# Kernel optimization log

Hardware: AMD Instinct MI355X
Metric: run time of the kernel (lower is better)

## Reference

```python
import jax, jax.numpy as jnp
import numpy as np

G, N, E = 4, 50000, 800000
F_IN, HID, OUT = 64, 128, 64


def setup_inputs() -> dict:
    key = jax.random.key(0)
    ks = jax.random.split(key, 4)
    x = jax.random.normal(ks[0], (G, N, F_IN), dtype=jnp.float32)
    edge_index = jax.random.randint(ks[1], (G, 2, E), 0, N)
    W1 = jax.random.normal(ks[2], (G, F_IN, HID), dtype=jnp.float32) / np.sqrt(F_IN).astype(np.float32)
    b1 = jnp.zeros((G, HID), dtype=jnp.float32)
    W2 = jax.random.normal(ks[3], (G, HID, OUT), dtype=jnp.float32) / np.sqrt(HID).astype(np.float32)
    b2 = jnp.zeros((G, OUT), dtype=jnp.float32)
    return {"x": x, "edge_index": edge_index, "W1": W1, "b1": b1, "W2": W2, "b2": b2}


def gcn_conv(x, src, dst, W, b):
    # PyG GCNConv: add self loops, symmetric norm D^-1/2 (A+I) D^-1/2, then XW + b
    n = x.shape[0]
    loop = jnp.arange(n)
    s = jnp.concatenate([src, loop])  # [E+N]
    d = jnp.concatenate([dst, loop])
    deg = jax.ops.segment_sum(jnp.ones_like(s, dtype=x.dtype), d, num_segments=n)
    dinv = jax.lax.rsqrt(deg)  # deg >= 1 because of self loops
    norm = dinv[s] * dinv[d]  # [E+N]
    h = x @ W  # [N, F_out]
    msg = h[s] * norm[:, None]  # edge-wise gather (memory-bound)
    out = jax.ops.segment_sum(msg, d, num_segments=n)  # scatter-add
    return out + b


def reference(x, edge_index, W1, b1, W2, b2):
    def per_graph(xg, eg, w1, b1g, w2, b2g):
        src, dst = eg[0], eg[1]
        h = jax.nn.elu(gcn_conv(xg, src, dst, w1, b1g))
        h = jax.nn.elu(gcn_conv(h, src, dst, w2, b2g))
        return h  # [N, OUT]

    out = jax.vmap(per_graph)(x, edge_index, W1, b1, W2, b2)  # [G, N, OUT]
    return out.reshape(G * N, OUT)  # torch.cat over graphs along dim 0
```

## Files before the change

### kernel.cpp

```cpp
#include <hip/hip_runtime.h>
#include <cstdint>

constexpr int G = 4, N = 50000, E = 800000;
constexpr int FIN = 64, HID = 128, FOUT = 64;
constexpr int NB = (N + 1023) / 1024;

constexpr int PB = 64;
constexpr int CP = E / PB;
constexpr int NBK = (N + 255) / 256;

typedef unsigned short ushort;
typedef _Float16 f16;

__device__ __forceinline__ ushort f2h(float f) {
  f16 h = (f16)f;
  return __builtin_bit_cast(ushort, h);
}
__device__ __forceinline__ float h2f(ushort u) {
  f16 h = __builtin_bit_cast(f16, u);
  return (float)h;
}

__device__ __forceinline__ void xcd_map(int b, int& g, int& chunk) {
  int xcd = b & 7;
  int sub = b >> 3;
  g = xcd >> 1;
  chunk = (xcd & 1) * 6250 + sub;
}

__global__ void k_x2h(const float4* __restrict__ X, ushort4* __restrict__ Xh, int n4) {
  int i = blockIdx.x * blockDim.x + threadIdx.x;
  if (i >= n4) return;
  float4 v = X[i];
  ushort4 o = {f2h(v.x), f2h(v.y), f2h(v.z), f2h(v.w)};
  Xh[i] = o;
}


__global__ __launch_bounds__(256) void k_phist(const int* __restrict__ ei,
                                               int* __restrict__ PH) {
  __shared__ int h[NBK];
  int pb = blockIdx.x, g = blockIdx.y;
  for (int i = threadIdx.x; i < NBK; i += 256) h[i] = 0;
  __syncthreads();
  const int4* dst4 = (const int4*)(ei + (size_t)g * 2 * E + E + (size_t)pb * CP);
  for (int i = threadIdx.x; i < CP / 4; i += 256) {
    int4 d = dst4[i];
    atomicAdd(&h[d.x >> 8], 1);
    atomicAdd(&h[d.y >> 8], 1);
    atomicAdd(&h[d.z >> 8], 1);
    atomicAdd(&h[d.w >> 8], 1);
  }
  __syncthreads();
  for (int i = threadIdx.x; i < NBK; i += 256)
    PH[((size_t)g * NBK + i) * PB + pb] = h[i];
}

__global__ void k_pscan(const int* __restrict__ PH, int* __restrict__ POFF,
                        int* __restrict__ BB) {
  int g = blockIdx.x, k = threadIdx.x;
  int tot = 0;
  if (k < NBK) {
#pragma unroll 8
    for (int pb = 0; pb < PB; ++pb) tot += PH[((size_t)g * NBK + k) * PB + pb];
  }
  __shared__ int sm[256];
  sm[k] = tot;
  __syncthreads();
  for (int off = 1; off < 256; off <<= 1) {
    int v = (k >= off) ? sm[k - off] : 0;
    __syncthreads();
    sm[k] += v;
    __syncthreads();
  }
  int excl = sm[k] - tot;
  if (k < NBK) {
    BB[g * (NBK + 1) + k] = excl;
    if (k == NBK - 1) BB[g * (NBK + 1) + NBK] = excl + tot;
    int run = excl;
#pragma unroll 8
    for (int pb = 0; pb < PB; ++pb) {
      POFF[((size_t)g * NBK + k) * PB + pb] = run;
      run += PH[((size_t)g * NBK + k) * PB + pb];
    }
  }
}

__global__ __launch_bounds__(256) void k_part(const int* __restrict__ ei,
                                              const int* __restrict__ POFF,
                                              unsigned* __restrict__ pairs) {
  __shared__ int off[NBK];
  __shared__ int rk[NBK];
  int pb = blockIdx.x, g = blockIdx.y;
  for (int i = threadIdx.x; i < NBK; i += 256) {
    off[i] = POFF[((size_t)g * NBK + i) * PB + pb];
    rk[i] = 0;
  }
  __syncthreads();
  const int* base = ei + (size_t)g * 2 * E + (size_t)pb * CP;
  const int4* s4 = (const int4*)base;
  const int4* d4 = (const int4*)(base + E);
  unsigned* pg = pairs + (size_t)g * E;
  for (int i = threadIdx.x; i < CP / 4; i += 256) {
    int4 s = s4[i], d = d4[i];
    int sv[4] = {s.x, s.y, s.z, s.w};
    int dv[4] = {d.x, d.y, d.z, d.w};
#pragma unroll
    for (int k = 0; k < 4; ++k) {
      int b = dv[k] >> 8;
      int r = atomicAdd(&rk[b], 1);
      pg[off[b] + r] = (unsigned)sv[k] | ((unsigned)(dv[k] & 255) << 16);
    }
  }
}

__global__ __launch_bounds__(256) void k_bcnt(const unsigned* __restrict__ pairs,
                                              const int* __restrict__ BB,
                                              int* __restrict__ cnt) {
  __shared__ int h[256];
  int k = blockIdx.x, g = blockIdx.y;
  h[threadIdx.x] = 0;
  __syncthreads();
  int lo = BB[g * (NBK + 1) + k], hi = BB[g * (NBK + 1) + k + 1];
  const unsigned* pg = pairs + (size_t)g * E;
  for (int i = lo + (int)threadIdx.x; i < hi; i += 256)
    atomicAdd(&h[(pg[i] >> 16) & 255], 1);
  __syncthreads();
  int n0 = k << 8;
  int nn = min(256, N - n0);
  if ((int)threadIdx.x < nn) cnt[g * N + n0 + threadIdx.x] = h[threadIdx.x];
}

__global__ __launch_bounds__(256) void k_place(const unsigned* __restrict__ pairs,
                                               const int* __restrict__ BB,
                                               const int* __restrict__ rowptr,
                                               int* __restrict__ col) {
  __shared__ int rp[256];
  __shared__ int rk[256];
  int k = blockIdx.x, g = blockIdx.y;
  int n0 = k << 8;
  int nn = min(256, N - n0);
  if ((int)threadIdx.x < nn) rp[threadIdx.x] = rowptr[g * (N + 1) + n0 + threadIdx.x];
  rk[threadIdx.x] = 0;
  __syncthreads();
  int lo = BB[g * (NBK + 1) + k], hi = BB[g * (NBK + 1) + k + 1];
  const unsigned* pg = pairs + (size_t)g * E;
  int* cg = col + (size_t)g * E;
  for (int i = lo + (int)threadIdx.x; i < hi; i += 256) {
    unsigned p = pg[i];
    int dl = (p >> 16) & 255;
    int r = atomicAdd(&rk[dl], 1);
    cg[rp[dl] + r] = (int)(p & 0xffffu);
  }
}

__global__ void k_scan_partial(const int* __restrict__ cnt, int* __restrict__ part) {
  int g = blockIdx.y, b = blockIdx.x, tid = threadIdx.x;
  int base = b * 1024 + tid * 4;
  int s = 0;
#pragma unroll
  for (int k = 0; k < 4; ++k) {
    int i = base + k;
    if (i < N) s += cnt[g * N + i];
  }
  __shared__ int sm[256];
  sm[tid] = s;
  __syncthreads();
  for (int off = 128; off > 0; off >>= 1) {
    if (tid < off) sm[tid] += sm[tid + off];
    __syncthreads();
  }
  if (tid == 0) part[g * NB + b] = sm[0];
}

__global__ void k_scan_mid(int* __restrict__ part, int* __restrict__ rowptr) {
  int g = blockIdx.x;
  if (threadIdx.x != 0) return;
  int run = 0;
  for (int b = 0; b < NB; ++b) {
    int t = part[g * NB + b];
    part[g * NB + b] = run;
    run += t;
  }
  rowptr[g * (N + 1) + N] = run;
}

__global__ void k_scan_final(const int* __restrict__ cnt, const int* __restrict__ part,
                             int* __restrict__ rowptr, float* __restrict__ dinv) {
  int g = blockIdx.y, b = blockIdx.x, tid = threadIdx.x;
  int base = b * 1024 + tid * 4;
  int c[4];
  int s = 0;
#pragma unroll
  for (int k = 0; k < 4; ++k) {
    int i = base + k;
    c[k] = (i < N) ? cnt[g * N + i] : 0;
    s += c[k];
  }
  __shared__ int sm[256];
  sm[tid] = s;
  __syncthreads();
  for (int off = 1; off < 256; off <<= 1) {
    int v = (tid >= off) ? sm[tid - off] : 0;
    __syncthreads();
    sm[tid] += v;
    __syncthreads();
  }
  int excl = sm[tid] - s + part[g * NB + b];
#pragma unroll
  for (int k = 0; k < 4; ++k) {
    int i = base + k;
    if (i < N) {
      rowptr[g * (N + 1) + i] = excl;
      dinv[g * N + i] = rsqrtf((float)(c[k] + 1));
    }
    excl += c[k];
  }
}

template <int K, int F, bool PRESCALE, bool BIASELU, bool OUTH>
__global__ __launch_bounds__(256) void k_gemm_lds(const float* __restrict__ X,
                                                  const float* __restrict__ W,
                                                  const float* __restrict__ dinv,
                                                  const float* __restrict__ bias,
                                                  void* __restrict__ Hout) {
  constexpr int CH = F / 4;
  constexpr int PK = K + 1;
  __shared__ float xs[64 * PK];
  int g = blockIdx.y;
  int R0 = blockIdx.x * 64;
  for (int idx = threadIdx.x; idx < 64 * K; idx += 256) {
    int r = idx / K, k = idx - r * K;
    int row = R0 + r;
    xs[r * PK + k] = (row < N) ? X[((size_t)g * N + row) * K + k] : 0.f;
  }
  __syncthreads();
  int wv = threadIdx.x >> 6;
  int lane = threadIdx.x & 63;
  int c0 = __builtin_amdgcn_readfirstlane(wv * CH);
  const float* Wg = W + (size_t)g * K * F;
  const float* xrow = &xs[lane * PK];
  float acc[CH];
#pragma unroll
  for (int c = 0; c < CH; ++c) acc[c] = 0.f;
#pragma unroll 4
  for (int k = 0; k < K; ++k) {
    float xv = xrow[k];
#pragma unroll
    for (int c = 0; c < CH; ++c)
      acc[c] = fmaf(xv, Wg[(size_t)k * F + c0 + c], acc[c]);
  }
  int row = R0 + lane;
  if (row >= N) return;
  if constexpr (PRESCALE) {
    float sc = dinv[g * N + row];
#pragma unroll
    for (int c = 0; c < CH; ++c) acc[c] *= sc;
  }
  if constexpr (BIASELU) {
#pragma unroll
    for (int c = 0; c < CH; ++c) {
      float v = acc[c] + bias[g * F + c0 + c];
      acc[c] = v > 0.f ? v : expm1f(v);
    }
  }
  if constexpr (OUTH) {
    ushort* opb = (ushort*)Hout + ((size_t)g * N + row) * F + c0;
#pragma unroll
    for (int c4 = 0; c4 < CH; c4 += 4) {
      ushort4 o = {f2h(acc[c4]), f2h(acc[c4 + 1]), f2h(acc[c4 + 2]),
                   f2h(acc[c4 + 3])};
      *(ushort4*)(opb + c4) = o;
    }
  } else {
    float* op = (float*)Hout + ((size_t)g * N + row) * F + c0;
#pragma unroll
    for (int c4 = 0; c4 < CH; c4 += 4) {
      float4 o = {acc[c4], acc[c4 + 1], acc[c4 + 2], acc[c4 + 3]};
      *(float4*)(op + c4) = o;
    }
  }
}

template <int F>
__global__ __launch_bounds__(256) void k_agg_in(const ushort* __restrict__ Xh,
                                                const int* __restrict__ rowptr,
                                                const int* __restrict__ col,
                                                const float* __restrict__ dinv,
                                                float* __restrict__ Z) {
  int g, chunk;
  xcd_map(blockIdx.x, g, chunk);
  int d = chunk * 4 + (threadIdx.x >> 6);
  int lane = threadIdx.x & 63;
  const ushort* hb = Xh + (size_t)g * N * F;
  const float* dv = dinv + g * N;
  const int* cl = col + (size_t)g * E;
  int rs = rowptr[g * (N + 1) + d];
  int re = rowptr[g * (N + 1) + d + 1];
  float dd = dv[d];
  float acc = dd * h2f(hb[(size_t)d * F + lane]);
  for (int j0 = rs; j0 < re; j0 += 64) {
    int idx = j0 + lane;
    int myc = (idx < re) ? cl[idx] : 0;
    float myd = (idx < re) ? dv[myc] : 0.f;
    int nn = min(64, re - j0);
    int jj = 0;
    for (; jj + 8 <= nn; jj += 8) {
      int s[8];
      float sw[8];
#pragma unroll
      for (int k = 0; k < 8; ++k) {
        s[k] = __shfl(myc, jj + k, 64);
        sw[k] = __shfl(myd, jj + k, 64);
      }
      float v[8];
#pragma unroll
      for (int k = 0; k < 8; ++k) v[k] = h2f(hb[(size_t)s[k] * F + lane]);
#pragma unroll
      for (int k = 0; k < 8; ++k) acc += sw[k] * v[k];
    }
    for (; jj < nn; ++jj) {
      int s = __shfl(myc, jj, 64);
      float sw = __shfl(myd, jj, 64);
      acc += sw * h2f(hb[(size_t)s * F + lane]);
    }
  }
  Z[((size_t)g * N + d) * F + lane] = dd * acc;
}

template <int F>
__global__ __launch_bounds__(256) void k_agg_out(const ushort* __restrict__ Hsrc,
                                                 const int* __restrict__ rowptr,
                                                 const int* __restrict__ col,
                                                 const float* __restrict__ dinv,
                                                 const float* __restrict__ bias,
                                                 float* __restrict__ out) {
  int g, chunk;
  xcd_map(blockIdx.x, g, chunk);
  int d = chunk * 4 + (threadIdx.x >> 6);
  int lane = threadIdx.x & 63;
  const ushort* hb = Hsrc + (size_t)g * N * F;
  const int* cl = col + (size_t)g * E;
  int rs = rowptr[g * (N + 1) + d];
  int re = rowptr[g * (N + 1) + d + 1];
  float acc = h2f(hb[(size_t)d * F + lane]);
  for (int j0 = rs; j0 < re; j0 += 64) {
    int idx = j0 + lane;
    int myc = (idx < re) ? cl[idx] : 0;
    int nn = min(64, re - j0);
    int jj = 0;
    for (; jj + 8 <= nn; jj += 8) {
      int s[8];
#pragma unroll
      for (int k = 0; k < 8; ++k) s[k] = __shfl(myc, jj + k, 64);
      float v[8];
#pragma unroll
      for (int k = 0; k < 8; ++k) v[k] = h2f(hb[(size_t)s[k] * F + lane]);
#pragma unroll
      for (int k = 0; k < 8; ++k) acc += v[k];
    }
    for (; jj < nn; ++jj) {
      int s = __shfl(myc, jj, 64);
      acc += h2f(hb[(size_t)s * F + lane]);
    }
  }
  float p = acc * dinv[g * N + d] + bias[g * F + lane];
  p = p > 0.f ? p : expm1f(p);
  out[((size_t)g * N + d) * F + lane] = p;
}

extern "C" void kernel_launch(void* const* d_in, const int* in_sizes, int n_in,
                              void* d_out, int out_size, void* d_ws, size_t ws_size,
                              hipStream_t stream) {
  const float* x = (const float*)d_in[0];
  const int* ei = (const int*)d_in[1];
  const float* W1 = (const float*)d_in[2];
  const float* b1 = (const float*)d_in[3];
  const float* W2 = (const float*)d_in[4];
  const float* b2 = (const float*)d_in[5];
  float* out = (float*)d_out;

  char* p = (char*)d_ws;
  auto alloc = [&](size_t bytes) {
    char* r = p;
    p += (bytes + 255) & ~(size_t)255;
    return r;
  };
  int* cnt = (int*)alloc(sizeof(int) * G * N);
  int* rowptr = (int*)alloc(sizeof(int) * G * (N + 1));
  int* part = (int*)alloc(sizeof(int) * G * NB);
  float* dinv = (float*)alloc(sizeof(float) * G * N);
  int* col = (int*)alloc(sizeof(int) * (size_t)G * E);
  float* z = (float*)alloc(sizeof(float) * (size_t)G * N * FIN);
  float* h1 = (float*)alloc(sizeof(float) * (size_t)G * N * HID);
  ushort* h2s = (ushort*)z;
  unsigned* pairs = (unsigned*)h1;
  int* PH = (int*)((char*)h1 + ((size_t)13 << 20));
  int* POFF = (int*)((char*)h1 + ((size_t)14 << 20));
  int* BB = (int*)((char*)h1 + ((size_t)15 << 20));
  ushort* xh = (ushort*)((char*)h1 + ((size_t)32 << 20));

  k_x2h<<<(G * N * FIN / 4 + 255) / 256, 256, 0, stream>>>((const float4*)x,
                                                           (ushort4*)xh, G * N * FIN / 4);

  k_phist<<<dim3(PB, G), 256, 0, stream>>>(ei, PH);
  k_pscan<<<G, 256, 0, stream>>>(PH, POFF, BB);
  k_part<<<dim3(PB, G), 256, 0, stream>>>(ei, POFF, pairs);
  k_bcnt<<<dim3(NBK, G), 256, 0, stream>>>(pairs, BB, cnt);
  dim3 sg(NB, G);
  k_scan_partial<<<sg, 256, 0, stream>>>(cnt, part);
  k_scan_mid<<<G, 64, 0, stream>>>(part, rowptr);
  k_scan_final<<<sg, 256, 0, stream>>>(cnt, part, rowptr, dinv);
  k_place<<<dim3(NBK, G), 256, 0, stream>>>(pairs, BB, rowptr, col);

  k_agg_in<FIN><<<(G * N) / 4, 256, 0, stream>>>(xh, rowptr, col, dinv, z);
  dim3 gg((N + 63) / 64, G);
  k_gemm_lds<FIN, HID, false, true, false>
      <<<gg, 256, 0, stream>>>(z, W1, nullptr, b1, h1);

  k_gemm_lds<HID, FOUT, true, false, true>
      <<<gg, 256, 0, stream>>>(h1, W2, dinv, nullptr, h2s);
  k_agg_out<FOUT><<<(G * N) / 4, 256, 0, stream>>>(h2s, rowptr, col, dinv, b2, out);
}
```

Before: 544.5 us.

## Prescale fp16 features by dinv and read edge indices as wave-uniform scalar loads

Result: faster. 525.2 us (-3.5%).

```diff
diff --git a/kernel.cpp b/kernel.cpp
--- a/kernel.cpp
+++ b/kernel.cpp
@@ -28,11 +28,13 @@
   chunk = (xcd & 1) * 6250 + sub;
 }
 
-__global__ void k_x2h(const float4* __restrict__ X, ushort4* __restrict__ Xh, int n4) {
+__global__ void k_x2h(const float4* __restrict__ X, const float* __restrict__ dinv,
+                      ushort4* __restrict__ Xh, int n4) {
   int i = blockIdx.x * blockDim.x + threadIdx.x;
   if (i >= n4) return;
+  float sc = dinv[i >> 4];
   float4 v = X[i];
-  ushort4 o = {f2h(v.x), f2h(v.y), f2h(v.z), f2h(v.w)};
+  ushort4 o = {f2h(sc * v.x), f2h(sc * v.y), f2h(sc * v.z), f2h(sc * v.w)};
   Xh[i] = o;
 }
 
@@ -290,42 +292,26 @@
                                                 float* __restrict__ Z) {
   int g, chunk;
   xcd_map(blockIdx.x, g, chunk);
-  int d = chunk * 4 + (threadIdx.x >> 6);
+  int d = __builtin_amdgcn_readfirstlane(chunk * 4 + (threadIdx.x >> 6));
   int lane = threadIdx.x & 63;
   const ushort* hb = Xh + (size_t)g * N * F;
-  const float* dv = dinv + g * N;
   const int* cl = col + (size_t)g * E;
   int rs = rowptr[g * (N + 1) + d];
   int re = rowptr[g * (N + 1) + d + 1];
-  float dd = dv[d];
-  float acc = dd * h2f(hb[(size_t)d * F + lane]);
-  for (int j0 = rs; j0 < re; j0 += 64) {
-    int idx = j0 + lane;
-    int myc = (idx < re) ? cl[idx] : 0;
-    float myd = (idx < re) ? dv[myc] : 0.f;
-    int nn = min(64, re - j0);
-    int jj = 0;
-    for (; jj + 8 <= nn; jj += 8) {
-      int s[8];
-      float sw[8];
-#pragma unroll
-      for (int k = 0; k < 8; ++k) {
-        s[k] = __shfl(myc, jj + k, 64);
-        sw[k] = __shfl(myd, jj + k, 64);
-      }
-      float v[8];
-#pragma unroll
-      for (int k = 0; k < 8; ++k) v[k] = h2f(hb[(size_t)s[k] * F + lane]);
-#pragma unroll
-      for (int k = 0; k < 8; ++k) acc += sw[k] * v[k];
-    }
-    for (; jj < nn; ++jj) {
-      int s = __shfl(myc, jj, 64);
-      float sw = __shfl(myd, jj, 64);
-      acc += sw * h2f(hb[(size_t)s * F + lane]);
-    }
-  }
-  Z[((size_t)g * N + d) * F + lane] = dd * acc;
+  float acc = h2f(hb[(size_t)d * F + lane]);
+  int j = rs;
+  for (; j + 8 <= re; j += 8) {
+    int s[8];
+#pragma unroll
+    for (int k = 0; k < 8; ++k) s[k] = cl[j + k];
+    float v[8];
+#pragma unroll
+    for (int k = 0; k < 8; ++k) v[k] = h2f(hb[(size_t)s[k] * F + lane]);
+#pragma unroll
+    for (int k = 0; k < 8; ++k) acc += v[k];
+  }
+  for (; j < re; ++j) acc += h2f(hb[(size_t)cl[j] * F + lane]);
+  Z[((size_t)g * N + d) * F + lane] = dinv[g * N + d] * acc;
 }
 
 template <int F>
@@ -337,33 +323,25 @@
                                                  float* __restrict__ out) {
   int g, chunk;
   xcd_map(blockIdx.x, g, chunk);
-  int d = chunk * 4 + (threadIdx.x >> 6);
+  int d = __builtin_amdgcn_readfirstlane(chunk * 4 + (threadIdx.x >> 6));
   int lane = threadIdx.x & 63;
   const ushort* hb = Hsrc + (size_t)g * N * F;
   const int* cl = col + (size_t)g * E;
   int rs = rowptr[g * (N + 1) + d];
   int re = rowptr[g * (N + 1) + d + 1];
   float acc = h2f(hb[(size_t)d * F + lane]);
-  for (int j0 = rs; j0 < re; j0 += 64) {
-    int idx = j0 + lane;
-    int myc = (idx < re) ? cl[idx] : 0;
-    int nn = min(64, re - j0);
-    int jj = 0;
-    for (; jj + 8 <= nn; jj += 8) {
-      int s[8];
-#pragma unroll
-      for (int k = 0; k < 8; ++k) s[k] = __shfl(myc, jj + k, 64);
-      float v[8];
-#pragma unroll
-      for (int k = 0; k < 8; ++k) v[k] = h2f(hb[(size_t)s[k] * F + lane]);
-#pragma unroll
-      for (int k = 0; k < 8; ++k) acc += v[k];
-    }
-    for (; jj < nn; ++jj) {
-      int s = __shfl(myc, jj, 64);
-      acc += h2f(hb[(size_t)s * F + lane]);
-    }
-  }
+  int j = rs;
+  for (; j + 8 <= re; j += 8) {
+    int s[8];
+#pragma unroll
+    for (int k = 0; k < 8; ++k) s[k] = cl[j + k];
+    float v[8];
+#pragma unroll
+    for (int k = 0; k < 8; ++k) v[k] = h2f(hb[(size_t)s[k] * F + lane]);
+#pragma unroll
+    for (int k = 0; k < 8; ++k) acc += v[k];
+  }
+  for (; j < re; ++j) acc += h2f(hb[(size_t)cl[j] * F + lane]);
   float p = acc * dinv[g * N + d] + bias[g * F + lane];
   p = p > 0.f ? p : expm1f(p);
   out[((size_t)g * N + d) * F + lane] = p;
@@ -400,9 +378,6 @@
   int* BB = (int*)((char*)h1 + ((size_t)15 << 20));
   ushort* xh = (ushort*)((char*)h1 + ((size_t)32 << 20));
 
-  k_x2h<<<(G * N * FIN / 4 + 255) / 256, 256, 0, stream>>>((const float4*)x,
-                                                           (ushort4*)xh, G * N * FIN / 4);
-
   k_phist<<<dim3(PB, G), 256, 0, stream>>>(ei, PH);
   k_pscan<<<G, 256, 0, stream>>>(PH, POFF, BB);
   k_part<<<dim3(PB, G), 256, 0, stream>>>(ei, POFF, pairs);
@@ -413,6 +388,9 @@
   k_scan_final<<<sg, 256, 0, stream>>>(cnt, part, rowptr, dinv);
   k_place<<<dim3(NBK, G), 256, 0, stream>>>(pairs, BB, rowptr, col);
 
+  k_x2h<<<(G * N * FIN / 4 + 255) / 256, 256, 0, stream>>>(
+      (const float4*)x, dinv, (ushort4*)xh, G * N * FIN / 4);
+
   k_agg_in<FIN><<<(G * N) / 4, 256, 0, stream>>>(xh, rowptr, col, dinv, z);
   dim3 gg((N + 63) / 64, G);
   k_gemm_lds<FIN, HID, false, true, false>
```
